# Optimization experiments

Measured on AMD Instinct MI355X. Metric: run time of the kernel, lower is better.

The kernel has to match this reference:

```python
import jax, jax.numpy as jnp
import numpy as np


def _hard_softmax(w):
    # w: (O, I, K, K). One-hot at the abs-argmax of each output row (eval path).
    O = w.shape[0]
    flat = jnp.abs(w).reshape(O, -1)
    idx = jnp.argmax(flat, axis=1)
    oh = jax.nn.one_hot(idx, flat.shape[1], dtype=w.dtype)
    return oh.reshape(w.shape)


def setup_inputs() -> dict:
    key = jax.random.key(0)
    k1, k2 = jax.random.split(key)
    B, C, H, W = 16, 64, 256, 256
    x = jax.random.normal(k1, (B, C, H, W), dtype=jnp.float32)
    weight = jax.random.normal(k2, (1, 1, 3, 3), dtype=jnp.float32)
    return {"x": x, "weight": weight}


def reference(x, weight):
    C = x.shape[1]
    w_hard = _hard_softmax(weight).astype(x.dtype)      # (1,1,3,3) one-hot
    w_rep = jnp.tile(w_hard, (C, 1, 1, 1))              # (C,1,3,3) depthwise kernel
    out = jax.lax.conv_general_dilated(
        x, w_rep,
        window_strides=(1, 1),
        padding=((1, 1), (1, 1)),
        feature_group_count=C,
        dimension_numbers=("NCHW", "OIHW", "NCHW"),
    )
    return out
```

## Files before the change

kernel.cpp:

```cpp
#include <hip/hip_runtime.h>


__global__ __launch_bounds__(256) void ShiftConvGeneral_65738769433039_kernel(
    const float* __restrict__ x, const float* __restrict__ w,
    float* __restrict__ out) {
    __shared__ int s_sh, s_sw;
    if (threadIdx.x == 0) {
        float best = -1.0f;
        int bi = 0;
#pragma unroll
        for (int i = 0; i < 9; ++i) {
            float a = fabsf(w[i]);
            if (a > best) { best = a; bi = i; }
        }
        s_sh = bi / 3 - 1;
        s_sw = bi % 3 - 1;
    }
    __syncthreads();
    const int sh = s_sh;
    const int sw = s_sw;

    const int tid  = threadIdx.x;
    const int lane = tid & 63;
    const int row_global = blockIdx.x * 4 + (tid >> 6);
    const int h   = row_global & 255;
    const int img = row_global >> 8;
    const int c0  = lane << 2;

    const int hin = h + sh;
    float4 v = make_float4(0.f, 0.f, 0.f, 0.f);
    if ((unsigned)hin < 256u) {
        const float* in_row = x + ((size_t)img << 16) + ((size_t)hin << 8);
        if (sw == 0) {
            v = *(const float4*)(in_row + c0);
        } else {
            float r[4];
#pragma unroll
            for (int j = 0; j < 4; ++j) {
                int cc = c0 + sw + j;
                r[j] = ((unsigned)cc < 256u) ? in_row[cc] : 0.f;
            }
            v = make_float4(r[0], r[1], r[2], r[3]);
        }
    }
    float4* orow = (float4*)(out + ((size_t)row_global << 8));
    orow[lane] = v;
}

extern "C" void kernel_launch(void* const* d_in, const int* in_sizes, int n_in,
                              void* d_out, int out_size, void* d_ws, size_t ws_size,
                              hipStream_t stream) {
    const float* x = (const float*)d_in[0];
    const float* w = (const float*)d_in[1];
    float* out = (float*)d_out;

    const int total_rows = 16 * 64 * 256;
    const int blocks = total_rows / 4;
    ShiftConvGeneral_65738769433039_kernel<<<blocks, 256, 0, stream>>>(x, w, out);
}
```

Baseline: 414.9 us.

## Split shift selection into prep kernel and stream rows with nontemporal vector copies

Moves the abs-argmax shift computation into a one-thread prep kernel that writes to workspace, which removes the per-block serial argmax and __syncthreads. The copy kernel now handles 32 rows per block and uses nontemporal float4 loads and stores. Horizontal shifts are done with a wavefront shuffle instead of four scalar unaligned loads. This adds a second kernel launch and fewer blocks, for a copy that is bandwidth-bound at about 268MB each way.

```diff
diff --git a/kernel.cpp b/kernel.cpp
--- a/kernel.cpp
+++ b/kernel.cpp
@@ -1,10 +1,10 @@
 #include <hip/hip_runtime.h>
 
 
-__global__ __launch_bounds__(256) void ShiftConvGeneral_65738769433039_kernel(
-    const float* __restrict__ x, const float* __restrict__ w,
-    float* __restrict__ out) {
-    __shared__ int s_sh, s_sw;
+typedef float v4f __attribute__((ext_vector_type(4)));
+
+__global__ void shift_prep_kernel(const float* __restrict__ w,
+                                  int* __restrict__ shifts) {
     if (threadIdx.x == 0) {
         float best = -1.0f;
         int bi = 0;
@@ -13,38 +13,49 @@
             float a = fabsf(w[i]);
             if (a > best) { best = a; bi = i; }
         }
-        s_sh = bi / 3 - 1;
-        s_sw = bi % 3 - 1;
+        shifts[0] = bi / 3 - 1;
+        shifts[1] = bi % 3 - 1;
     }
-    __syncthreads();
-    const int sh = s_sh;
-    const int sw = s_sw;
+}
 
-    const int tid  = threadIdx.x;
-    const int lane = tid & 63;
-    const int row_global = blockIdx.x * 4 + (tid >> 6);
-    const int h   = row_global & 255;
-    const int img = row_global >> 8;
-    const int c0  = lane << 2;
+#define ROWS_PER_BLOCK 32
 
-    const int hin = h + sh;
-    float4 v = make_float4(0.f, 0.f, 0.f, 0.f);
-    if ((unsigned)hin < 256u) {
-        const float* in_row = x + ((size_t)img << 16) + ((size_t)hin << 8);
-        if (sw == 0) {
-            v = *(const float4*)(in_row + c0);
-        } else {
-            float r[4];
+__global__ __launch_bounds__(256) void shift_copy_kernel(
+    const float* __restrict__ x, const int* __restrict__ shifts,
+    float* __restrict__ out) {
+    const int sh = shifts[0];
+    const int sw = shifts[1];
+    const int lane = threadIdx.x & 63;
+    const int wid  = threadIdx.x >> 6;
+
+    const int block_row0 = blockIdx.x * ROWS_PER_BLOCK;
+    const int img = block_row0 >> 8;
+    const int h_base = block_row0 & 255;
+    const float* __restrict__ xin  = x   + ((size_t)img << 16);
+    float*       __restrict__ oimg = out + ((size_t)img << 16);
+
 #pragma unroll
-            for (int j = 0; j < 4; ++j) {
-                int cc = c0 + sw + j;
-                r[j] = ((unsigned)cc < 256u) ? in_row[cc] : 0.f;
+    for (int it = 0; it < ROWS_PER_BLOCK / 4; ++it) {
+        const int h = h_base + it * 4 + wid;
+        const int hin = h + sh;
+        v4f v = {0.f, 0.f, 0.f, 0.f};
+        if ((unsigned)hin < 256u) {
+            const v4f* inq = (const v4f*)(xin + ((size_t)hin << 8));
+            v4f q = __builtin_nontemporal_load(inq + lane);
+            if (sw == 0) {
+                v = q;
+            } else if (sw == 1) {
+                float nb = __shfl_down(q.x, 1);
+                v.x = q.y; v.y = q.z; v.z = q.w;
+                v.w = (lane == 63) ? 0.f : nb;
+            } else {
+                float nb = __shfl_up(q.w, 1);
+                v.y = q.x; v.z = q.y; v.w = q.z;
+                v.x = (lane == 0) ? 0.f : nb;
             }
-            v = make_float4(r[0], r[1], r[2], r[3]);
         }
+        __builtin_nontemporal_store(v, (v4f*)(oimg + ((size_t)h << 8)) + lane);
     }
-    float4* orow = (float4*)(out + ((size_t)row_global << 8));
-    orow[lane] = v;
 }
 
 extern "C" void kernel_launch(void* const* d_in, const int* in_sizes, int n_in,
@@ -53,8 +64,11 @@
     const float* x = (const float*)d_in[0];
     const float* w = (const float*)d_in[1];
     float* out = (float*)d_out;
+    int* shifts = (int*)d_ws;
+
+    shift_prep_kernel<<<1, 64, 0, stream>>>(w, shifts);
 
     const int total_rows = 16 * 64 * 256;
-    const int blocks = total_rows / 4;
-    ShiftConvGeneral_65738769433039_kernel<<<blocks, 256, 0, stream>>>(x, w, out);
+    const int blocks = total_rows / ROWS_PER_BLOCK;
+    shift_copy_kernel<<<blocks, 256, 0, stream>>>(x, shifts, out);
 }
```

Result: slower. 425.5 us (+2.6%).
